# Performance work log

Measured on AMD Instinct MI355X. Metric: run time of the kernel, lower is better.

The kernel has to match this reference:

```python
import jax, jax.numpy as jnp
import numpy as np

N_NODES = 100000
N_EDGES = 1600000
D_FEAT = 64
H1 = 16
H2 = 1


def setup_inputs() -> dict:
    key = jax.random.key(0)
    ks = jax.random.split(key, 8)
    x = jax.random.normal(ks[0], (N_NODES, D_FEAT), dtype=jnp.float32)
    edge_index = jax.random.randint(ks[1], (2, N_EDGES), 0, N_NODES, dtype=jnp.int64)
    s1 = 1.0 / np.sqrt(D_FEAT)
    s2 = 1.0 / np.sqrt(H1)
    Wl1 = jax.random.uniform(ks[2], (H1, D_FEAT), jnp.float32, -s1, s1)
    Wr1 = jax.random.uniform(ks[3], (H1, D_FEAT), jnp.float32, -s1, s1)
    b1 = jax.random.uniform(ks[4], (H1,), jnp.float32, -s1, s1)
    Wl2 = jax.random.uniform(ks[5], (H2, H1), jnp.float32, -s2, s2)
    Wr2 = jax.random.uniform(ks[6], (H2, H1), jnp.float32, -s2, s2)
    b2 = jax.random.uniform(ks[7], (H2,), jnp.float32, -s2, s2)
    return {"x": x, "edge_index": edge_index, "Wl1": Wl1, "Wr1": Wr1, "b1": b1,
            "Wl2": Wl2, "Wr2": Wr2, "b2": b2}


def _sage_conv(h, src, dst, Wl, Wr, b, n_nodes):
    # mean aggregation of source-node features onto destination nodes
    msg_sum = jax.ops.segment_sum(h[src], dst, num_segments=n_nodes)  # [N, d]
    cnt = jax.ops.segment_sum(jnp.ones((src.shape[0],), h.dtype), dst,
                              num_segments=n_nodes)  # [N]
    mean = msg_sum / jnp.maximum(cnt, 1.0)[:, None]
    # out = lin_l(mean_neighbors) + lin_r(self) + bias
    return mean @ Wl.T + h @ Wr.T + b


def reference(x, edge_index, Wl1, Wr1, b1, Wl2, Wr2, b2):
    src, dst = edge_index[0], edge_index[1]
    n = x.shape[0]
    h = jax.nn.relu(_sage_conv(x, src, dst, Wl1, Wr1, b1, n))
    # F.dropout(training=False) is identity at inference
    out = _sage_conv(h, src, dst, Wl2, Wr2, b2, n)
    return out
```

## Files before the change

kernel.cpp:

```cpp
#include <hip/hip_runtime.h>
#include <hip/hip_fp16.h>

#define H1F 16
#define BSH 8
#define BNODES 256
#define MAXBUCK 512
#define CAPSH 13
#define SSH 10
#define TILE 4096
#define MAXPT 16

struct Params {
    const float* x;
    const float* Wl1; const float* Wr1; const float* b1;
    const float* Wl2; const float* Wr2; const float* b2;
    const int* ei;
    int* cur8;
    unsigned int* edge2;
    int* csr; int* offp; int* degv;
    __half* xl; float* xr; float* hl2; float* outp;
    float* out;
    int N, E, nPart, nProj, nbuck;
};

union SharedU {
    struct {
        int lhist[MAXBUCK];
        int lbase[MAXBUCK];
        int gbase[MAXBUCK];
        int wsum[8];
        unsigned int stage[TILE];
        unsigned short sbuck[TILE];
    } p;
    struct {
        float4 wl4[16][17];
        float4 wr4[16][17];
    } q;
    struct {
        int h[BNODES];
        int wsum[4];
    } s;
};

__device__ __forceinline__ void do_part(const Params& P, int vb, SharedU& sh) {
    int t = threadIdx.x;
    int shard = vb & 7;
    sh.p.lhist[t] = 0;
    __syncthreads();

    int E = P.E;
    int e0 = vb * TILE;
    int eb = e0 + t * 8;

    int ss[8], dd[8];
    if (eb + 8 <= E) {
        int4 s0 = *(const int4*)(P.ei + eb);
        int4 s1 = *(const int4*)(P.ei + eb + 4);
        int4 d0 = *(const int4*)(P.ei + E + eb);
        int4 d1 = *(const int4*)(P.ei + E + eb + 4);
        ss[0]=s0.x; ss[1]=s0.y; ss[2]=s0.z; ss[3]=s0.w;
        ss[4]=s1.x; ss[5]=s1.y; ss[6]=s1.z; ss[7]=s1.w;
        dd[0]=d0.x; dd[1]=d0.y; dd[2]=d0.z; dd[3]=d0.w;
        dd[4]=d1.x; dd[5]=d1.y; dd[6]=d1.z; dd[7]=d1.w;
    } else {
#pragma unroll
        for (int k = 0; k < 8; ++k) {
            int e = eb + k;
            ss[k] = (e < E) ? P.ei[e] : -1;
            dd[k] = (e < E) ? P.ei[E + e] : 0;
        }
    }

    unsigned int pk[8];
    int rk[8], bk[8];
#pragma unroll
    for (int k = 0; k < 8; ++k) {
        if (ss[k] >= 0) {
            int b = dd[k] >> BSH;
            bk[k] = b;
            pk[k] = ((unsigned int)ss[k] << BSH) |
                    (unsigned int)(dd[k] & (BNODES - 1));
            rk[k] = atomicAdd(&sh.p.lhist[b], 1);
        } else {
            bk[k] = -1;
        }
    }
    __syncthreads();

    int cnt = E - e0; if (cnt > TILE) cnt = TILE;

    int v = sh.p.lhist[t];
    if (v > 0)
        sh.p.gbase[t] = (t << CAPSH) + (shard << SSH) +
                        atomicAdd(&P.cur8[shard * MAXBUCK + t], v);
    int lane = t & 63, wid = t >> 6;
    int s = v;
#pragma unroll
    for (int d = 1; d < 64; d <<= 1) {
        int u = __shfl_up(s, d);
        if (lane >= d) s += u;
    }
    if (lane == 63) sh.p.wsum[wid] = s;
    __syncthreads();
    int wofs = 0;
    for (int w = 0; w < wid; ++w) wofs += sh.p.wsum[w];
    sh.p.lbase[t] = wofs + s - v;
    __syncthreads();

#pragma unroll
    for (int k = 0; k < 8; ++k) {
        if (bk[k] >= 0) {
            int p = sh.p.lbase[bk[k]] + rk[k];
            sh.p.stage[p] = pk[k];
            sh.p.sbuck[p] = (unsigned short)bk[k];
        }
    }
    __syncthreads();

    for (int i = t; i < cnt; i += 512) {
        int b = sh.p.sbuck[i];
        int idx = sh.p.gbase[b] + (i - sh.p.lbase[b]);
        int shardEnd = (b << CAPSH) + ((shard + 1) << SSH);
        if (idx < shardEnd) P.edge2[idx] = sh.p.stage[i];
    }
}

__device__ __forceinline__ void do_proj(const Params& P, int pvb, SharedU& sh) {
    int t = threadIdx.x;
    if (t < 256) {
        sh.q.wl4[t >> 4][t & 15] = ((const float4*)P.Wl1)[t];
    } else {
        int u = t - 256;
        sh.q.wr4[u >> 4][u & 15] = ((const float4*)P.Wr1)[u];
    }
    __syncthreads();

    int f = t & 15;
    int nl = t >> 4;
    float bf = P.b1[f];
    const float4* x4 = (const float4*)P.x;

#pragma unroll
    for (int rep = 0; rep < 4; ++rep) {
        int gn = pvb * 128 + rep * 32 + nl;
        if (gn < P.N) {
            float al = 0.0f, ar = 0.0f;
#pragma unroll
            for (int k4 = 0; k4 < 16; ++k4) {
                float4 xv = x4[(size_t)gn * 16 + k4];
                float4 a = sh.q.wl4[f][k4];
                float4 b = sh.q.wr4[f][k4];
                al += xv.x * a.x + xv.y * a.y + xv.z * a.z + xv.w * a.w;
                ar += xv.x * b.x + xv.y * b.y + xv.z * b.z + xv.w * b.w;
            }
            P.xl[(size_t)gn * H1F + f] = __float2half(al);
            P.xr[(size_t)gn * H1F + f] = ar + bf;
        }
    }
}

__device__ __forceinline__ void do_sort(const Params& P, int b, SharedU& sh) {
    int t = threadIdx.x;
    int n0 = b << BSH;
    int e0 = b << CAPSH;

    if (t < BNODES) sh.s.h[t] = 0;
    __syncthreads();

    unsigned int rw[MAXPT];
#pragma unroll
    for (int s = 0; s < 8; ++s) {
        int cs = P.cur8[s * MAXBUCK + b];
        if (cs > (1 << SSH)) cs = (1 << SSH);
        int base = e0 + (s << SSH);
#pragma unroll
        for (int k = 0; k < 2; ++k) {
            int idx = (k << 9) + t;
            rw[s * 2 + k] = (idx < cs) ? P.edge2[base + idx] : 0xFFFFFFFFu;
        }
    }

#pragma unroll
    for (int k = 0; k < MAXPT; ++k)
        if (rw[k] != 0xFFFFFFFFu) atomicAdd(&sh.s.h[rw[k] & (BNODES - 1)], 1);
    __syncthreads();

    int lane = t & 63, wid = t >> 6;
    int v = 0, s = 0;
    if (t < BNODES) {
        v = sh.s.h[t];
        s = v;
#pragma unroll
        for (int d = 1; d < 64; d <<= 1) {
            int u = __shfl_up(s, d);
            if (lane >= d) s += u;
        }
        if (lane == 63) sh.s.wsum[wid] = s;
    }
    __syncthreads();
    if (t < BNODES) {
        int wofs = 0;
        for (int w = 0; w < wid; ++w) wofs += sh.s.wsum[w];
        int excl = wofs + s - v;
        int gn = n0 + t;
        if (gn < P.N) {
            P.degv[gn] = v;
            P.offp[gn] = e0 + excl;
        }
        sh.s.h[t] = excl;
    }
    __syncthreads();

#pragma unroll
    for (int k = 0; k < MAXPT; ++k) {
        if (rw[k] != 0xFFFFFFFFu) {
            int d = (int)(rw[k] & (BNODES - 1));
            int pos = atomicAdd(&sh.s.h[d], 1);
            P.csr[e0 + pos] = (int)(rw[k] >> BSH);
        }
    }
}

__device__ __forceinline__ void do_gather1(const Params& P, int vb) {
    int t = threadIdx.x;
    int node = vb * 64 + (t >> 3);
    int l = t & 7;
    if (node >= P.N) return;

    const __half2* xl2 = (const __half2*)P.xl;
    const float2* xr2 = (const float2*)P.xr;

    int d = P.degv[node];
    const int* row = P.csr + P.offp[node];

    float sx = 0.0f, sy = 0.0f;
    int j = 0;
    for (; j + 4 <= d; j += 4) {
        int s0 = row[j], s1 = row[j + 1], s2 = row[j + 2], s3 = row[j + 3];
        float2 v0 = __half22float2(xl2[(size_t)s0 * 8 + l]);
        float2 v1 = __half22float2(xl2[(size_t)s1 * 8 + l]);
        float2 v2 = __half22float2(xl2[(size_t)s2 * 8 + l]);
        float2 v3 = __half22float2(xl2[(size_t)s3 * 8 + l]);
        sx += v0.x + v1.x + v2.x + v3.x;
        sy += v0.y + v1.y + v2.y + v3.y;
    }
    for (; j < d; ++j) {
        float2 v = __half22float2(xl2[(size_t)row[j] * 8 + l]);
        sx += v.x; sy += v.y;
    }

    float inv = 1.0f / fmaxf((float)d, 1.0f);
    float2 xrv = xr2[(size_t)node * 8 + l];
    float h0 = fmaxf(sx * inv + xrv.x, 0.0f);
    float h1 = fmaxf(sy * inv + xrv.y, 0.0f);
    float2 wlv = ((const float2*)P.Wl2)[l];
    float2 wrv = ((const float2*)P.Wr2)[l];
    float pl = h0 * wlv.x + h1 * wlv.y;
    float pr = h0 * wrv.x + h1 * wrv.y;
#pragma unroll
    for (int off = 4; off; off >>= 1) {
        pl += __shfl_xor(pl, off);
        pr += __shfl_xor(pr, off);
    }
    if (l == 0) {
        P.hl2[node] = pl;
        P.outp[node] = pr + P.b2[0];
    }
}

__device__ __forceinline__ void do_gather2(const Params& P, int vb) {
    int t = threadIdx.x;
    int node = vb * 128 + (t >> 2);
    int l = t & 3;
    if (node >= P.N) return;

    int d = P.degv[node];
    const int* row = P.csr + P.offp[node];

    float s = 0.0f;
    for (int j = l; j < d; j += 4) s += P.hl2[row[j]];
    s += __shfl_xor(s, 1);
    s += __shfl_xor(s, 2);
    if (l == 0) P.out[node] = s / fmaxf((float)d, 1.0f) + P.outp[node];
}

__global__ __launch_bounds__(512) void kA(Params P) {
    __shared__ SharedU sh;
    int vb = blockIdx.x;
    if (vb < P.nPart) do_part(P, vb, sh);
    else do_proj(P, vb - P.nPart, sh);
}
__global__ __launch_bounds__(512) void kB(Params P) {
    __shared__ SharedU sh;
    do_sort(P, blockIdx.x, sh);
}
__global__ __launch_bounds__(512) void kC(Params P) { do_gather1(P, blockIdx.x); }
__global__ __launch_bounds__(512) void kD(Params P) { do_gather2(P, blockIdx.x); }

extern "C" void kernel_launch(void* const* d_in, const int* in_sizes, int n_in,
                              void* d_out, int out_size, void* d_ws, size_t ws_size,
                              hipStream_t stream) {
    Params P;
    P.x   = (const float*)d_in[0];
    P.ei  = (const int*)d_in[1];
    P.Wl1 = (const float*)d_in[2];
    P.Wr1 = (const float*)d_in[3];
    P.b1  = (const float*)d_in[4];
    P.Wl2 = (const float*)d_in[5];
    P.Wr2 = (const float*)d_in[6];
    P.b2  = (const float*)d_in[7];
    P.out = (float*)d_out;

    P.N = in_sizes[0] / 64;
    P.E = in_sizes[1] / 2;
    P.nbuck = (P.N + BNODES - 1) >> BSH;
    P.nPart = (P.E + TILE - 1) / TILE;
    P.nProj = (P.N + 127) / 128;

    size_t win = (size_t)P.nbuck << CAPSH;
    P.cur8  = (int*)d_ws;
    P.edge2 = (unsigned int*)(P.cur8 + 8 * MAXBUCK);
    P.csr   = (int*)(P.edge2 + win);
    P.offp  = P.csr + win;
    P.degv  = P.offp + P.N;
    P.xl    = (__half*)(P.degv + P.N);
    P.xr    = (float*)(P.xl + (size_t)16 * P.N);
    P.hl2   = P.xr + (size_t)16 * P.N;
    P.outp  = P.hl2 + P.N;

    (void)hipMemsetAsync(P.cur8, 0, 8 * MAXBUCK * sizeof(int), stream);

    kA<<<P.nPart + P.nProj, 512, 0, stream>>>(P);
    kB<<<P.nbuck, 512, 0, stream>>>(P);
    kC<<<(P.N + 63) / 64, 512, 0, stream>>>(P);
    kD<<<(P.N + 127) / 128, 512, 0, stream>>>(P);
}
```

Before: 76.83 us.

## Fuse bucket sort with first-layer gather using shared-memory CSR

Measured after the change: 68.01 us. 1.13x faster.

```diff
diff --git a/kernel.cpp b/kernel.cpp
--- a/kernel.cpp
+++ b/kernel.cpp
@@ -6,6 +6,7 @@
 #define BNODES 256
 #define MAXBUCK 512
 #define CAPSH 13
+#define CAPB (1 << CAPSH)
 #define SSH 10
 #define TILE 4096
 #define MAXPT 16
@@ -36,10 +37,6 @@
         float4 wl4[16][17];
         float4 wr4[16][17];
     } q;
-    struct {
-        int h[BNODES];
-        int wsum[4];
-    } s;
 };
 
 __device__ __forceinline__ void do_part(const Params& P, int vb, SharedU& sh) {
@@ -159,55 +156,73 @@
     }
 }
 
-__device__ __forceinline__ void do_sort(const Params& P, int b, SharedU& sh) {
+__global__ __launch_bounds__(512) void kA(Params P) {
+    __shared__ SharedU sh;
+    int vb = blockIdx.x;
+    if (vb < P.nPart) do_part(P, vb, sh);
+    else do_proj(P, vb - P.nPart, sh);
+}
+
+__global__ __launch_bounds__(512) void kBC(Params P) {
+    __shared__ int sorted[CAPB];
+    __shared__ int hh[BNODES];
+    __shared__ int ofs[BNODES];
+    __shared__ int dgs[BNODES];
+    __shared__ int wsum[4];
+
     int t = threadIdx.x;
+    int b = blockIdx.x;
     int n0 = b << BSH;
     int e0 = b << CAPSH;
 
-    if (t < BNODES) sh.s.h[t] = 0;
-    __syncthreads();
-
+    if (t < BNODES) hh[t] = 0;
+    __syncthreads();
+
+    int cnt = 0;
     unsigned int rw[MAXPT];
 #pragma unroll
     for (int s = 0; s < 8; ++s) {
-        int cs = P.cur8[s * MAXBUCK + b];
-        if (cs > (1 << SSH)) cs = (1 << SSH);
+        int c = P.cur8[s * MAXBUCK + b];
+        if (c > (1 << SSH)) c = (1 << SSH);
+        cnt += c;
         int base = e0 + (s << SSH);
 #pragma unroll
         for (int k = 0; k < 2; ++k) {
             int idx = (k << 9) + t;
-            rw[s * 2 + k] = (idx < cs) ? P.edge2[base + idx] : 0xFFFFFFFFu;
+            rw[s * 2 + k] = (idx < c) ? P.edge2[base + idx] : 0xFFFFFFFFu;
         }
     }
 
 #pragma unroll
     for (int k = 0; k < MAXPT; ++k)
-        if (rw[k] != 0xFFFFFFFFu) atomicAdd(&sh.s.h[rw[k] & (BNODES - 1)], 1);
+        if (rw[k] != 0xFFFFFFFFu) atomicAdd(&hh[rw[k] & (BNODES - 1)], 1);
     __syncthreads();
 
     int lane = t & 63, wid = t >> 6;
     int v = 0, s = 0;
     if (t < BNODES) {
-        v = sh.s.h[t];
+        v = hh[t];
         s = v;
 #pragma unroll
         for (int d = 1; d < 64; d <<= 1) {
             int u = __shfl_up(s, d);
             if (lane >= d) s += u;
         }
-        if (lane == 63) sh.s.wsum[wid] = s;
+        if (lane == 63) wsum[wid] = s;
     }
     __syncthreads();
     if (t < BNODES) {
         int wofs = 0;
-        for (int w = 0; w < wid; ++w) wofs += sh.s.wsum[w];
+        for (int w = 0; w < wid; ++w) wofs += wsum[w];
         int excl = wofs + s - v;
+        ofs[t] = excl;
+        dgs[t] = v;
         int gn = n0 + t;
         if (gn < P.N) {
             P.degv[gn] = v;
             P.offp[gn] = e0 + excl;
         }
-        sh.s.h[t] = excl;
+        hh[t] = excl;
     }
     __syncthreads();
 
@@ -215,62 +230,73 @@
     for (int k = 0; k < MAXPT; ++k) {
         if (rw[k] != 0xFFFFFFFFu) {
             int d = (int)(rw[k] & (BNODES - 1));
-            int pos = atomicAdd(&sh.s.h[d], 1);
-            P.csr[e0 + pos] = (int)(rw[k] >> BSH);
-        }
-    }
-}
-
-__device__ __forceinline__ void do_gather1(const Params& P, int vb) {
-    int t = threadIdx.x;
-    int node = vb * 64 + (t >> 3);
-    int l = t & 7;
-    if (node >= P.N) return;
+            int pos = atomicAdd(&hh[d], 1);
+            sorted[pos] = (int)(rw[k] >> BSH);
+        }
+    }
+    __syncthreads();
+
+    for (int i = t; i < cnt; i += 512) P.csr[e0 + i] = sorted[i];
 
     const __half2* xl2 = (const __half2*)P.xl;
     const float2* xr2 = (const float2*)P.xr;
-
-    int d = P.degv[node];
-    const int* row = P.csr + P.offp[node];
-
-    float sx = 0.0f, sy = 0.0f;
-    int j = 0;
-    for (; j + 4 <= d; j += 4) {
-        int s0 = row[j], s1 = row[j + 1], s2 = row[j + 2], s3 = row[j + 3];
-        float2 v0 = __half22float2(xl2[(size_t)s0 * 8 + l]);
-        float2 v1 = __half22float2(xl2[(size_t)s1 * 8 + l]);
-        float2 v2 = __half22float2(xl2[(size_t)s2 * 8 + l]);
-        float2 v3 = __half22float2(xl2[(size_t)s3 * 8 + l]);
-        sx += v0.x + v1.x + v2.x + v3.x;
-        sy += v0.y + v1.y + v2.y + v3.y;
-    }
-    for (; j < d; ++j) {
-        float2 v = __half22float2(xl2[(size_t)row[j] * 8 + l]);
-        sx += v.x; sy += v.y;
-    }
-
-    float inv = 1.0f / fmaxf((float)d, 1.0f);
-    float2 xrv = xr2[(size_t)node * 8 + l];
-    float h0 = fmaxf(sx * inv + xrv.x, 0.0f);
-    float h1 = fmaxf(sy * inv + xrv.y, 0.0f);
+    int l = t & 7;
+    int nb = t >> 3;
     float2 wlv = ((const float2*)P.Wl2)[l];
     float2 wrv = ((const float2*)P.Wr2)[l];
-    float pl = h0 * wlv.x + h1 * wlv.y;
-    float pr = h0 * wrv.x + h1 * wrv.y;
-#pragma unroll
-    for (int off = 4; off; off >>= 1) {
-        pl += __shfl_xor(pl, off);
-        pr += __shfl_xor(pr, off);
-    }
-    if (l == 0) {
-        P.hl2[node] = pl;
-        P.outp[node] = pr + P.b2[0];
-    }
-}
-
-__device__ __forceinline__ void do_gather2(const Params& P, int vb) {
+    float bias2 = P.b2[0];
+
+#pragma unroll
+    for (int sub = 0; sub < 4; ++sub) {
+        int nl = sub * 64 + nb;
+        int node = n0 + nl;
+        if (node < P.N) {
+            int start = ofs[nl];
+            int d = dgs[nl];
+            float sx = 0.0f, sy = 0.0f;
+            int j = 0;
+            for (; j + 4 <= d; j += 4) {
+                int s0 = sorted[start + j], s1 = sorted[start + j + 1];
+                int s2 = sorted[start + j + 2], s3 = sorted[start + j + 3];
+                float2 v0 = __half22float2(xl2[(size_t)s0 * 8 + l]);
+                float2 v1 = __half22float2(xl2[(size_t)s1 * 8 + l]);
+                float2 v2 = __half22float2(xl2[(size_t)s2 * 8 + l]);
+                float2 v3 = __half22float2(xl2[(size_t)s3 * 8 + l]);
+                sx += v0.x + v1.x + v2.x + v3.x;
+                sy += v0.y + v1.y + v2.y + v3.y;
+            }
+            for (; j < d; ++j) {
+                float2 vv = __half22float2(xl2[(size_t)sorted[start + j] * 8 + l]);
+                sx += vv.x; sy += vv.y;
+            }
+
+            float inv = 1.0f / fmaxf((float)d, 1.0f);
+            float2 xrv = xr2[(size_t)node * 8 + l];
+            float h0 = fmaxf(sx * inv + xrv.x, 0.0f);
+            float h1 = fmaxf(sy * inv + xrv.y, 0.0f);
+            float pl = h0 * wlv.x + h1 * wlv.y;
+            float pr = h0 * wrv.x + h1 * wrv.y;
+#pragma unroll
+            for (int off = 4; off; off >>= 1) {
+                pl += __shfl_xor(pl, off);
+                pr += __shfl_xor(pr, off);
+            }
+            if (l == 0) {
+                P.hl2[node] = pl;
+                P.outp[node] = pr + bias2;
+            }
+        }
+    }
+}
+
+__global__ __launch_bounds__(512) void kD(Params P) {
+    int g = blockIdx.x;
+    int xcd = g & 7, r = g >> 3;
+    int bi = r >> 1, k = r & 1;
+    int b = bi * 8 + xcd;
+    if (b >= P.nbuck) return;
     int t = threadIdx.x;
-    int node = vb * 128 + (t >> 2);
+    int node = (b << BSH) + (k << 7) + (t >> 2);
     int l = t & 3;
     if (node >= P.N) return;
 
@@ -283,19 +309,6 @@
     s += __shfl_xor(s, 2);
     if (l == 0) P.out[node] = s / fmaxf((float)d, 1.0f) + P.outp[node];
 }
-
-__global__ __launch_bounds__(512) void kA(Params P) {
-    __shared__ SharedU sh;
-    int vb = blockIdx.x;
-    if (vb < P.nPart) do_part(P, vb, sh);
-    else do_proj(P, vb - P.nPart, sh);
-}
-__global__ __launch_bounds__(512) void kB(Params P) {
-    __shared__ SharedU sh;
-    do_sort(P, blockIdx.x, sh);
-}
-__global__ __launch_bounds__(512) void kC(Params P) { do_gather1(P, blockIdx.x); }
-__global__ __launch_bounds__(512) void kD(Params P) { do_gather2(P, blockIdx.x); }
 
 extern "C" void kernel_launch(void* const* d_in, const int* in_sizes, int n_in,
                               void* d_out, int out_size, void* d_ws, size_t ws_size,
@@ -331,7 +344,7 @@
     (void)hipMemsetAsync(P.cur8, 0, 8 * MAXBUCK * sizeof(int), stream);
 
     kA<<<P.nPart + P.nProj, 512, 0, stream>>>(P);
-    kB<<<P.nbuck, 512, 0, stream>>>(P);
-    kC<<<(P.N + 63) / 64, 512, 0, stream>>>(P);
-    kD<<<(P.N + 127) / 128, 512, 0, stream>>>(P);
-}
+    kBC<<<P.nbuck, 512, 0, stream>>>(P);
+    int gridD = 8 * ((P.nbuck + 7) / 8) * 2;
+    kD<<<gridD, 512, 0, stream>>>(P);
+}
```
